# Performance work log

Measured on AMD Instinct MI355X. Metric: run time of the kernel, lower is better.

Reference implementation:

```python
import jax, jax.numpy as jnp
import numpy as np

B, T, D_IN, H, K, C = 8, 2048, 512, 384, 8192, 8
N_BLOCKS = 6
EPS = 1e-5


def conv1d(x, w, b, pad, groups=1):
    # x: [B, Cin, T], w: [Cout, Cin//groups, k]
    y = jax.lax.conv_general_dilated(
        x, w, window_strides=(1,), padding=[(pad, pad)],
        dimension_numbers=("NCH", "OIH", "NCH"), feature_group_count=groups)
    return y + b[None, :, None]


def layernorm(x, g, b):
    # normalize over last axis
    m = jnp.mean(x, axis=-1, keepdims=True)
    v = jnp.mean(jnp.square(x - m), axis=-1, keepdims=True)
    return (x - m) * jax.lax.rsqrt(v + EPS) * g + b


def setup_inputs() -> dict:
    key = jax.random.key(0)
    ks = iter(jax.random.split(key, 32))
    s = 0.02
    inp = {
        "x": jax.random.normal(next(ks), (B, T, D_IN), dtype=jnp.float32),
        "enc_w": jax.random.normal(next(ks), (H, D_IN, 7)) * s,
        "enc_b": jnp.zeros((H,)),
        "enc_ln_g": jnp.ones((H,)),
        "enc_ln_b": jnp.zeros((H,)),
        "blk_dw_w": jax.random.normal(next(ks), (N_BLOCKS, H, 1, 7)) * s,
        "blk_dw_b": jnp.zeros((N_BLOCKS, H)),
        "blk_ln_g": jnp.ones((N_BLOCKS, H)),
        "blk_ln_b": jnp.zeros((N_BLOCKS, H)),
        "blk_w1": jax.random.normal(next(ks), (N_BLOCKS, 4 * H, H)) * s,
        "blk_b1": jnp.zeros((N_BLOCKS, 4 * H)),
        "blk_w2": jax.random.normal(next(ks), (N_BLOCKS, H, 4 * H)) * s,
        "blk_b2": jnp.zeros((N_BLOCKS, H)),
        "out_w": jax.random.normal(next(ks), (C, H, 1)) * s,
        "out_b": jnp.zeros((C,)),
        "embeddings": jax.random.normal(next(ks), (K, C)),
    }
    return inp


def encode(x, enc_w, enc_b, enc_ln_g, enc_ln_b, blk_dw_w, blk_dw_b,
           blk_ln_g, blk_ln_b, blk_w1, blk_b1, blk_w2, blk_b2, out_w, out_b):
    h = x.transpose(0, 2, 1)                       # [B, D_IN, T]
    h = conv1d(h, enc_w, enc_b, pad=3)             # [B, H, T]
    h = layernorm(h.transpose(0, 2, 1), enc_ln_g, enc_ln_b).transpose(0, 2, 1)
    for i in range(N_BLOCKS):
        res = h
        h = conv1d(h, blk_dw_w[i], blk_dw_b[i], pad=3, groups=H)  # depthwise
        ht = h.transpose(0, 2, 1)                  # [B, T, H]
        ht = layernorm(ht, blk_ln_g[i], blk_ln_b[i])
        ht = jnp.einsum("bth,fh->btf", ht, blk_w1[i]) + blk_b1[i]
        ht = jax.nn.gelu(ht, approximate=False)    # torch GELU is exact erf
        ht = jnp.einsum("btf,hf->bth", ht, blk_w2[i]) + blk_b2[i]
        h = ht.transpose(0, 2, 1) + res
    z = conv1d(h, out_w, out_b, pad=0)             # [B, C, T]
    return z.transpose(0, 2, 1)                    # [B, T, C]


def reference(x, enc_w, enc_b, enc_ln_g, enc_ln_b, blk_dw_w, blk_dw_b,
              blk_ln_g, blk_ln_b, blk_w1, blk_b1, blk_w2, blk_b2,
              out_w, out_b, embeddings):
    z = encode(x, enc_w, enc_b, enc_ln_g, enc_ln_b, blk_dw_w, blk_dw_b,
               blk_ln_g, blk_ln_b, blk_w1, blk_b1, blk_w2, blk_b2, out_w, out_b)
    flat = z.reshape(-1, C)                        # [B*T, C]
    # squared euclidean distances: same argmin as torch.cdist
    d2 = (jnp.sum(flat * flat, axis=1, keepdims=True)
          - 2.0 * flat @ embeddings.T
          + jnp.sum(embeddings * embeddings, axis=1))  # [B*T, K]
    indices = jnp.argmin(d2, axis=1)               # [B*T], int
    return indices
```

## Files before the change

kernel.cpp:

```cpp
#include <hip/hip_runtime.h>
#include <math.h>

#define T_   2048
#define DIN  512
#define H_   384
#define H4_  1536
#define BT_  16384

typedef _Float16 half_t;
typedef _Float16 f16x8 __attribute__((ext_vector_type(8)));
typedef _Float16 f16x4 __attribute__((ext_vector_type(4)));
typedef float f32x4 __attribute__((ext_vector_type(4)));

#define LO_SCALE 2048.0f
#define LO_INV   4.8828125e-4f

__device__ __forceinline__ void gload_lds(const half_t* g, half_t* l) {
    __builtin_amdgcn_global_load_lds(
        (const __attribute__((address_space(1))) unsigned int*)(const void*)g,
        (__attribute__((address_space(3))) unsigned int*)(void*)l, 16, 0, 0);
}

__device__ __forceinline__ void split2(float v, half_t* hi, half_t* lo) {
    half_t h = (half_t)v;
    *hi = h;
    *lo = (half_t)((v - (float)h) * LO_SCALE);
}

__global__ void k_split4(const float* __restrict__ in, half_t* __restrict__ hi,
                         half_t* __restrict__ lo, long n4) {
    long i = (long)blockIdx.x * 256 + threadIdx.x;
    if (i >= n4) return;
    float4 v = ((const float4*)in)[i];
    f16x4 vh, vl;
    float a[4] = {v.x, v.y, v.z, v.w};
#pragma unroll
    for (int j = 0; j < 4; ++j) {
        half_t h = (half_t)a[j];
        vh[j] = h;
        vl[j] = (half_t)((a[j] - (float)h) * LO_SCALE);
    }
    ((f16x4*)hi)[i] = vh;
    ((f16x4*)lo)[i] = vl;
}

__global__ void k_split_pad(const float* __restrict__ in, half_t* __restrict__ hi,
                            half_t* __restrict__ lo) {
    long i = (long)blockIdx.x * 256 + threadIdx.x;
    if (i >= 2103296L) return;
    int ii4 = (int)(i & 127);
    long rest = i >> 7;
    int u = (int)(rest % 2054);
    int b = (int)(rest / 2054);
    f16x4 vh = (f16x4)(half_t)0.f, vl = (f16x4)(half_t)0.f;
    if (u >= 3 && u < 2051) {
        float4 v = ((const float4*)in)[((long)b * 2048 + (u - 3)) * 128 + ii4];
        float a[4] = {v.x, v.y, v.z, v.w};
#pragma unroll
        for (int j = 0; j < 4; ++j) {
            half_t h = (half_t)a[j];
            vh[j] = h;
            vl[j] = (half_t)((a[j] - (float)h) * LO_SCALE);
        }
    }
    ((f16x4*)hi)[i] = vh;
    ((f16x4*)lo)[i] = vl;
}

__global__ void k_split_encw(const float* __restrict__ in, half_t* __restrict__ hi,
                             half_t* __restrict__ lo) {
    int idx = blockIdx.x * 256 + threadIdx.x;
    if (idx >= H_ * 3584) return;
    int n = idx / 3584;
    int r = idx % 3584;
    int tap = r >> 9, i = r & 511;
    split2(in[n * 3584 + i * 7 + tap], hi + idx, lo + idx);
}

__global__ void k_ln(const float* __restrict__ in, float* __restrict__ out,
                     const float* __restrict__ g, const float* __restrict__ b) {
    int row = blockIdx.x;
    int lane = threadIdx.x;
    const float* ir = in + (long)row * H_;
    float v[6];
    float s = 0.f;
#pragma unroll
    for (int j = 0; j < 6; ++j) { v[j] = ir[lane + (j << 6)]; s += v[j]; }
#pragma unroll
    for (int o = 32; o > 0; o >>= 1) s += __shfl_down(s, o, 64);
    s = __shfl(s, 0, 64);
    float mean = s * (1.f / 384.f);
    float q = 0.f;
#pragma unroll
    for (int j = 0; j < 6; ++j) { float d = v[j] - mean; q += d * d; }
#pragma unroll
    for (int o = 32; o > 0; o >>= 1) q += __shfl_down(q, o, 64);
    q = __shfl(q, 0, 64);
    float rstd = rsqrtf(q * (1.f / 384.f) + 1e-5f);
    float* orow = out + (long)row * H_;
#pragma unroll
    for (int j = 0; j < 6; ++j) {
        int c = lane + (j << 6);
        orow[c] = (v[j] - mean) * rstd * g[c] + b[c];
    }
}

__global__ __launch_bounds__(256) void k_dwconv_ln(
    const float* __restrict__ h, half_t* __restrict__ oh,
    half_t* __restrict__ ol,
    const float* __restrict__ w, const float* __restrict__ wb,
    const float* __restrict__ g, const float* __restrict__ gb) {
    int row = (blockIdx.x << 2) + (threadIdx.x >> 6);
    int b = row >> 11;
    int t = row & 2047;
    int lane = threadIdx.x & 63;
    const float* hb = h + ((long)b * T_) * H_;
    float vx[3], vy[3];
    float s = 0.f;
#pragma unroll
    for (int j = 0; j < 3; ++j) {
        int c = (lane << 1) + (j << 7);
        float ax = wb[c], ay = wb[c + 1];
        const float* wcx = w + c * 7;
        const float* wcy = wcx + 7;
#pragma unroll
        for (int k = 0; k < 7; ++k) {
            int tt = t + k - 3;
            if ((unsigned)tt < (unsigned)T_) {
                float2 hv = *(const float2*)&hb[(long)tt * H_ + c];
                ax = fmaf(hv.x, wcx[k], ax);
                ay = fmaf(hv.y, wcy[k], ay);
            }
        }
        vx[j] = ax; vy[j] = ay;
        s += ax + ay;
    }
#pragma unroll
    for (int o = 32; o > 0; o >>= 1) s += __shfl_down(s, o, 64);
    s = __shfl(s, 0, 64);
    float mean = s * (1.f / 384.f);
    float q = 0.f;
#pragma unroll
    for (int j = 0; j < 3; ++j) {
        float dx = vx[j] - mean, dy = vy[j] - mean;
        q += dx * dx + dy * dy;
    }
#pragma unroll
    for (int o = 32; o > 0; o >>= 1) q += __shfl_down(q, o, 64);
    q = __shfl(q, 0, 64);
    float rstd = rsqrtf(q * (1.f / 384.f) + 1e-5f);
    long ro = (long)row * H_;
#pragma unroll
    for (int j = 0; j < 3; ++j) {
        int c = (lane << 1) + (j << 7);
        float valx = (vx[j] - mean) * rstd * g[c] + gb[c];
        float valy = (vy[j] - mean) * rstd * g[c + 1] + gb[c + 1];
        split2(valx, oh + ro + c, ol + ro + c);
        split2(valy, oh + ro + c + 1, ol + ro + c + 1);
    }
}

template <int MODE, int NT>
__global__ __launch_bounds__(512, 2) void k_g192p(
    const half_t* __restrict__ Ah, const half_t* __restrict__ Al,
    const half_t* __restrict__ Bh, const half_t* __restrict__ Bl,
    const float* __restrict__ bias, const float* __restrict__ res,
    float* __restrict__ Cf, half_t* __restrict__ Ch, half_t* __restrict__ Cl,
    int N, int K) {
    __shared__ __align__(16) half_t smem[61440];
    const int tid = threadIdx.x;
    const int lane = tid & 63, wid = tid >> 6;
    const int wm = (wid & 1) << 6;
    const int wn = ((wid >> 1) & 3) * 48;
    const int quad = lane >> 4, l16 = lane & 15;

    constexpr int NWG = 128 * NT;
    constexpr int CHUNK = NWG / 8;
    const int lin = blockIdx.x;
    const int tile = (lin & 7) * CHUNK + (lin >> 3);
    const int m0 = (tile / NT) << 7;
    const int n0 = (tile % NT) * 192;

    long abase;
    int astr;
    if (MODE == 0) {
        abase = (long)(m0 >> 11) * 2054 + (m0 & 2047);
        astr = 512;
    } else {
        abase = m0;
        astr = K;
    }

    const int lr = lane >> 2;
    const int lg = (lane & 3) ^ ((lane >> 3) & 3);
    const half_t* gsrc[5];
    int ldo[5];
#pragma unroll
    for (int j = 0; j < 5; ++j) {
        int q = wid * 5 + j;
        if (q < 8) {
            gsrc[j] = Ah + (abase + q * 16 + lr) * (long)astr + lg * 8;
            ldo[j] = q * 512;
        } else if (q < 16) {
            gsrc[j] = Al + (abase + (q - 8) * 16 + lr) * (long)astr + lg * 8;
            ldo[j] = 4096 + (q - 8) * 512;
        } else if (q < 28) {
            gsrc[j] = Bh + ((long)(n0 + (q - 16) * 16 + lr)) * K + lg * 8;
            ldo[j] = 8192 + (q - 16) * 512;
        } else {
            gsrc[j] = Bl + ((long)(n0 + (q - 28) * 16 + lr)) * K + lg * 8;
            ldo[j] = 14336 + (q - 28) * 512;
        }
    }

#define STAGE3(bufb, k0_) do {                                              \
    int k0v = (k0_);                                                        \
    _Pragma("unroll")                                                       \
    for (int j = 0; j < 5; ++j)                                             \
        gload_lds(gsrc[j] + k0v, &smem[(bufb) + ldo[j]]);                   \
} while (0)

    f32x4 acc1[4][3] = {};
    f32x4 acc2[4][3] = {};
    const int sw = ((quad ^ (l16 >> 1)) & 3) << 3;

    const int nIter = K >> 5;
    STAGE3(0, 0);
    STAGE3(20480, 32);
    int b0 = 0, b1 = 20480, b2 = 40960;
    for (int it = 0; it < nIter; ++it) {
        if (it + 1 < nIter)
            asm volatile("s_waitcnt vmcnt(5)" ::: "memory");
        else
            asm volatile("s_waitcnt vmcnt(0)" ::: "memory");
        __builtin_amdgcn_s_barrier();
        __builtin_amdgcn_sched_barrier(0);

        const int ab = b0 + (wm + l16) * 32 + sw;
        const int bb = b0 + 8192 + (wn + l16) * 32 + sw;
        const int k2 = (it + 2) << 5;
        const bool st = (it + 2 < nIter);
        f16x8 fah[4], fal[4], fgh[3], fgl[3];

#pragma unroll
        for (int f = 0; f < 4; ++f)
            fah[f] = *(const f16x8*)&smem[ab + f * 512];
#pragma unroll
        for (int g = 0; g < 3; ++g)
            fgl[g] = *(const f16x8*)&smem[bb + 6144 + g * 512];
        if (st) {
            gload_lds(gsrc[0] + k2, &smem[b2 + ldo[0]]);
            gload_lds(gsrc[1] + k2, &smem[b2 + ldo[1]]);
        }
        __builtin_amdgcn_s_setprio(1);
#pragma unroll
        for (int f = 0; f < 4; ++f)
#pragma unroll
            for (int g = 0; g < 3; ++g)
                acc2[f][g] = __builtin_amdgcn_mfma_f32_16x16x32_f16(fah[f], fgl[g], acc2[f][g], 0, 0, 0);
        __builtin_amdgcn_s_setprio(0);

#pragma unroll
        for (int f = 0; f < 4; ++f)
            fal[f] = *(const f16x8*)&smem[ab + 4096 + f * 512];
#pragma unroll
        for (int g = 0; g < 3; ++g)
            fgh[g] = *(const f16x8*)&smem[bb + g * 512];
        if (st) {
            gload_lds(gsrc[2] + k2, &smem[b2 + ldo[2]]);
            gload_lds(gsrc[3] + k2, &smem[b2 + ldo[3]]);
            gload_lds(gsrc[4] + k2, &smem[b2 + ldo[4]]);
        }
        __builtin_amdgcn_s_setprio(1);
#pragma unroll
        for (int f = 0; f < 4; ++f)
#pragma unroll
            for (int g = 0; g < 3; ++g)
                acc2[f][g] = __builtin_amdgcn_mfma_f32_16x16x32_f16(fal[f], fgh[g], acc2[f][g], 0, 0, 0);
        __builtin_amdgcn_s_setprio(0);

        __builtin_amdgcn_s_setprio(1);
#pragma unroll
        for (int f = 0; f < 4; ++f)
#pragma unroll
            for (int g = 0; g < 3; ++g)
                acc1[f][g] = __builtin_amdgcn_mfma_f32_16x16x32_f16(fah[f], fgh[g], acc1[f][g], 0, 0, 0);
        __builtin_amdgcn_s_setprio(0);

        int t_ = b0; b0 = b1; b1 = b2; b2 = t_;
    }
#undef STAGE3

    float bv[3];
#pragma unroll
    for (int g = 0; g < 3; ++g) bv[g] = bias[n0 + wn + g * 16 + l16];

    if (MODE == 1) {
        __syncthreads();
#pragma unroll
        for (int f = 0; f < 4; ++f)
#pragma unroll
            for (int g = 0; g < 3; ++g)
#pragma unroll
                for (int r = 0; r < 4; ++r) {
                    int rm = wm + f * 16 + quad * 4 + r;
                    int cn = wn + g * 16 + l16;
                    float v = acc1[f][g][r] + acc2[f][g][r] * LO_INV + bv[g];
                    v = 0.5f * v * (1.0f + erff(v * 0.70710678118654752f));
                    half_t hh = (half_t)v;
                    smem[rm * 200 + cn] = hh;
                    smem[25600 + rm * 200 + cn] = (half_t)((v - (float)hh) * LO_SCALE);
                }
        __syncthreads();
        int row = tid >> 2, c0 = (tid & 3) * 48;
        long go = (long)(m0 + row) * N + n0 + c0;
        int so = row * 200 + c0;
#pragma unroll
        for (int u = 0; u < 6; ++u) {
            *(float4*)(Ch + go + u * 8) = *(const float4*)&smem[so + u * 8];
            *(float4*)(Cl + go + u * 8) = *(const float4*)&smem[25600 + so + u * 8];
        }
    } else {
#pragma unroll
        for (int f = 0; f < 4; ++f)
#pragma unroll
            for (int g = 0; g < 3; ++g)
#pragma unroll
                for (int r = 0; r < 4; ++r) {
                    long row = m0 + wm + f * 16 + quad * 4 + r;
                    int col = n0 + wn + g * 16 + l16;
                    float v = acc1[f][g][r] + acc2[f][g][r] * LO_INV + bv[g];
                    long o = row * N + col;
                    if (MODE == 2) v += res[o];
                    Cf[o] = v;
                }
    }
}

__global__ __launch_bounds__(256) void k_outconv_argmin(
    const float* __restrict__ h, const float* __restrict__ ow,
    const float* __restrict__ ob, const float* __restrict__ emb,
    int* __restrict__ outIdx) {
    __shared__ float hs[16][H_ + 1];
    __shared__ float zs[16][8];
    __shared__ float es[16 * 516];
    __shared__ float rb[16][16];
    __shared__ int ri[16][16];
    const int tid = threadIdx.x;
    const int row0 = blockIdx.x << 4;

    for (int i = tid; i < 16 * (H_ / 4); i += 256) {
        int r = i / 96;
        int c4 = (i % 96) << 2;
        float4 v = *(const float4*)&h[((long)(row0 + r)) * H_ + c4];
        hs[r][c4] = v.x; hs[r][c4 + 1] = v.y; hs[r][c4 + 2] = v.z; hs[r][c4 + 3] = v.w;
    }
    __syncthreads();

    if (tid < 128) {
        int r = tid & 15, c = tid >> 4;
        float acc = ob[c];
        const float* wc = ow + c * H_;
        for (int j = 0; j < H_; ++j) acc = fmaf(hs[r][j], wc[j], acc);
        zs[r][c] = acc;
    }
    __syncthreads();

    const int r = tid & 15;
    const int sl = tid >> 4;
    float z0 = zs[r][0], z1 = zs[r][1], z2 = zs[r][2], z3 = zs[r][3];
    float z4 = zs[r][4], z5 = zs[r][5], z6 = zs[r][6], z7 = zs[r][7];
    float best = 3.4e38f;
    int bi = 0;

    for (int ch = 0; ch < 8; ++ch) {
        __syncthreads();
        for (int i = tid; i < 2048; i += 256) {
            int e = i >> 1;
            int half = (i & 1) << 2;
            float4 src = *(const float4*)&emb[(((long)(ch << 10)) + e) * 8 + half];
            *(float4*)&es[(e >> 6) * 516 + ((e & 63) << 3) + half] = src;
        }
        __syncthreads();
        const float* ep = es + sl * 516;
        int gbase = (ch << 10) + (sl << 6);
#pragma unroll 4
        for (int j = 0; j < 64; ++j) {
            float4 e0 = *(const float4*)(ep + (j << 3));
            float4 e1 = *(const float4*)(ep + (j << 3) + 4);
            float t, d;
            t = e0.x - z0; d = t * t;
            t = e0.y - z1; d = fmaf(t, t, d);
            t = e0.z - z2; d = fmaf(t, t, d);
            t = e0.w - z3; d = fmaf(t, t, d);
            t = e1.x - z4; d = fmaf(t, t, d);
            t = e1.y - z5; d = fmaf(t, t, d);
            t = e1.z - z6; d = fmaf(t, t, d);
            t = e1.w - z7; d = fmaf(t, t, d);
            if (d < best) { best = d; bi = gbase + j; }
        }
    }
    rb[r][sl] = best;
    ri[r][sl] = bi;
    __syncthreads();
    if (sl == 0) {
        float bb = rb[r][0];
        int bbi = ri[r][0];
#pragma unroll
        for (int s2 = 1; s2 < 16; ++s2) {
            float v = rb[r][s2];
            int i2 = ri[r][s2];
            if (v < bb || (v == bb && i2 < bbi)) { bb = v; bbi = i2; }
        }
        outIdx[row0 + r] = bbi;
    }
}

extern "C" void kernel_launch(void* const* d_in, const int* in_sizes, int n_in,
                              void* d_out, int out_size, void* d_ws, size_t ws_size,
                              hipStream_t stream) {
    const float* x        = (const float*)d_in[0];
    const float* enc_w    = (const float*)d_in[1];
    const float* enc_b    = (const float*)d_in[2];
    const float* enc_ln_g = (const float*)d_in[3];
    const float* enc_ln_b = (const float*)d_in[4];
    const float* blk_dw_w = (const float*)d_in[5];
    const float* blk_dw_b = (const float*)d_in[6];
    const float* blk_ln_g = (const float*)d_in[7];
    const float* blk_ln_b = (const float*)d_in[8];
    const float* blk_w1   = (const float*)d_in[9];
    const float* blk_b1   = (const float*)d_in[10];
    const float* blk_w2   = (const float*)d_in[11];
    const float* blk_b2   = (const float*)d_in[12];
    const float* out_w    = (const float*)d_in[13];
    const float* out_b    = (const float*)d_in[14];
    const float* emb      = (const float*)d_in[15];
    int* out = (int*)d_out;

    char* base = (char*)d_ws;
    float*  h    = (float*)base;
    half_t* tmph = (half_t*)(base + 25165824);
    half_t* tmpl = (half_t*)(base + 37748736);
    half_t* ht4h = (half_t*)(base + 50331648);
    half_t* ht4l = (half_t*)(base + 100663296);
    half_t* ench = (half_t*)(base + 150994944);
    half_t* encl = (half_t*)(base + 153747456);
    half_t* w1h  = (half_t*)(base + 156499968);
    half_t* w1l  = (half_t*)(base + 163577856);
    half_t* w2h  = (half_t*)(base + 170655744);
    half_t* w2l  = (half_t*)(base + 177733632);
    half_t* xph = (half_t*)(base + 50331648);
    half_t* xpl = (half_t*)(base + 50331648 + 16826368);

    k_split_pad<<<8216, 256, 0, stream>>>(x, xph, xpl);
    k_split4<<<3456, 256, 0, stream>>>(blk_w1, w1h, w1l, 884736L);
    k_split4<<<3456, 256, 0, stream>>>(blk_w2, w2h, w2l, 884736L);
    k_split_encw<<<(H_ * 3584 + 255) / 256, 256, 0, stream>>>(enc_w, ench, encl);

    k_g192p<0, 2><<<256, 512, 0, stream>>>(xph, xpl, ench, encl, enc_b,
                                           nullptr, h, nullptr, nullptr,
                                           H_, 3584);
    k_ln<<<BT_, 64, 0, stream>>>(h, h, enc_ln_g, enc_ln_b);

    for (int i = 0; i < 6; ++i) {
        k_dwconv_ln<<<BT_ / 4, 256, 0, stream>>>(h, tmph, tmpl, blk_dw_w + i * H_ * 7,
                                                 blk_dw_b + i * H_, blk_ln_g + i * H_,
                                                 blk_ln_b + i * H_);
        k_g192p<1, 8><<<1024, 512, 0, stream>>>(
            tmph, tmpl, w1h + (long)i * 589824, w1l + (long)i * 589824,
            blk_b1 + i * H4_, nullptr, nullptr, ht4h, ht4l, H4_, H_);
        k_g192p<2, 2><<<256, 512, 0, stream>>>(
            ht4h, ht4l, w2h + (long)i * 589824, w2l + (long)i * 589824,
            blk_b2 + i * H_, h, h, nullptr, nullptr, H_, H4_);
    }

    k_outconv_argmin<<<BT_ / 16, 256, 0, stream>>>(h, out_w, out_b, emb, out);
}
```

Before: 1.647 ms.

## Stage GEMM epilogue through LDS, stagger wave LDS reads, batch LN rows

The fp32 GEMM epilogue (modes 0 and 2) now writes accumulators to padded LDS, then each thread stores 48 contiguous floats with float4 writes and float4 residual reads, replacing scattered per-element global accesses. The second group of waves reverses the order of its hi/lo fragment loads inside the main loop, which is meant to spread LDS bank and port pressure across waves. The standalone layernorm kernel now handles four rows per 256-thread block instead of one row per 64-thread block. The epilogue adds two barriers and reuses LDS that the pipeline also uses.

```diff
diff --git a/kernel.cpp b/kernel.cpp
--- a/kernel.cpp
+++ b/kernel.cpp
@@ -77,10 +77,11 @@
     split2(in[n * 3584 + i * 7 + tap], hi + idx, lo + idx);
 }
 
-__global__ void k_ln(const float* __restrict__ in, float* __restrict__ out,
-                     const float* __restrict__ g, const float* __restrict__ b) {
-    int row = blockIdx.x;
-    int lane = threadIdx.x;
+__global__ __launch_bounds__(256) void k_ln(
+    const float* __restrict__ in, float* __restrict__ out,
+    const float* __restrict__ g, const float* __restrict__ b) {
+    int row = (blockIdx.x << 2) + (threadIdx.x >> 6);
+    int lane = threadIdx.x & 63;
     const float* ir = in + (long)row * H_;
     float v[6];
     float s = 0.f;
@@ -159,6 +160,57 @@
         split2(valy, oh + ro + c + 1, ol + ro + c + 1);
     }
 }
+
+#define KHALF1(AOFF, BOFF, F1A, F1B)                                        \
+    _Pragma("unroll")                                                       \
+    for (int f = 0; f < 4; ++f)                                             \
+        F1A[f] = *(const f16x8*)&smem[ab + (AOFF) + f * 512];               \
+    _Pragma("unroll")                                                       \
+    for (int g = 0; g < 3; ++g)                                             \
+        F1B[g] = *(const f16x8*)&smem[bb + (BOFF) + g * 512];               \
+    if (st) {                                                               \
+        gload_lds(gsrc[0] + k2, &smem[b2 + ldo[0]]);                        \
+        gload_lds(gsrc[1] + k2, &smem[b2 + ldo[1]]);                        \
+    }                                                                       \
+    __builtin_amdgcn_s_setprio(1);                                          \
+    _Pragma("unroll")                                                       \
+    for (int f = 0; f < 4; ++f)                                             \
+        _Pragma("unroll")                                                   \
+        for (int g = 0; g < 3; ++g)                                         \
+            acc2[f][g] = __builtin_amdgcn_mfma_f32_16x16x32_f16(            \
+                F1A[f], F1B[g], acc2[f][g], 0, 0, 0);                       \
+    __builtin_amdgcn_s_setprio(0);
+
+#define KHALF2(AOFF, BOFF, F2A, F2B)                                        \
+    _Pragma("unroll")                                                       \
+    for (int f = 0; f < 4; ++f)                                             \
+        F2A[f] = *(const f16x8*)&smem[ab + (AOFF) + f * 512];               \
+    _Pragma("unroll")                                                       \
+    for (int g = 0; g < 3; ++g)                                             \
+        F2B[g] = *(const f16x8*)&smem[bb + (BOFF) + g * 512];               \
+    if (st) {                                                               \
+        gload_lds(gsrc[2] + k2, &smem[b2 + ldo[2]]);                        \
+        gload_lds(gsrc[3] + k2, &smem[b2 + ldo[3]]);                        \
+        gload_lds(gsrc[4] + k2, &smem[b2 + ldo[4]]);                        \
+    }                                                                       \
+    __builtin_amdgcn_s_setprio(1);                                          \
+    _Pragma("unroll")                                                       \
+    for (int f = 0; f < 4; ++f)                                             \
+        _Pragma("unroll")                                                   \
+        for (int g = 0; g < 3; ++g)                                         \
+            acc2[f][g] = __builtin_amdgcn_mfma_f32_16x16x32_f16(            \
+                F2A[f], F2B[g], acc2[f][g], 0, 0, 0);                       \
+    __builtin_amdgcn_s_setprio(0);
+
+#define KHI(FAH, FGH)                                                       \
+    __builtin_amdgcn_s_setprio(1);                                          \
+    _Pragma("unroll")                                                       \
+    for (int f = 0; f < 4; ++f)                                             \
+        _Pragma("unroll")                                                   \
+        for (int g = 0; g < 3; ++g)                                         \
+            acc1[f][g] = __builtin_amdgcn_mfma_f32_16x16x32_f16(            \
+                FAH[f], FGH[g], acc1[f][g], 0, 0, 0);                       \
+    __builtin_amdgcn_s_setprio(0);
 
 template <int MODE, int NT>
 __global__ __launch_bounds__(512, 2) void k_g192p(
@@ -173,6 +225,7 @@
     const int wm = (wid & 1) << 6;
     const int wn = ((wid >> 1) & 3) * 48;
     const int quad = lane >> 4, l16 = lane & 15;
+    const bool flip = (wid >> 2) & 1;
 
     constexpr int NWG = 128 * NT;
     constexpr int CHUNK = NWG / 8;
@@ -240,52 +293,18 @@
         const int bb = b0 + 8192 + (wn + l16) * 32 + sw;
         const int k2 = (it + 2) << 5;
         const bool st = (it + 2 < nIter);
-        f16x8 fah[4], fal[4], fgh[3], fgl[3];
-
-#pragma unroll
-        for (int f = 0; f < 4; ++f)
-            fah[f] = *(const f16x8*)&smem[ab + f * 512];
-#pragma unroll
-        for (int g = 0; g < 3; ++g)
-            fgl[g] = *(const f16x8*)&smem[bb + 6144 + g * 512];
-        if (st) {
-            gload_lds(gsrc[0] + k2, &smem[b2 + ldo[0]]);
-            gload_lds(gsrc[1] + k2, &smem[b2 + ldo[1]]);
-        }
-        __builtin_amdgcn_s_setprio(1);
-#pragma unroll
-        for (int f = 0; f < 4; ++f)
-#pragma unroll
-            for (int g = 0; g < 3; ++g)
-                acc2[f][g] = __builtin_amdgcn_mfma_f32_16x16x32_f16(fah[f], fgl[g], acc2[f][g], 0, 0, 0);
-        __builtin_amdgcn_s_setprio(0);
-
-#pragma unroll
-        for (int f = 0; f < 4; ++f)
-            fal[f] = *(const f16x8*)&smem[ab + 4096 + f * 512];
-#pragma unroll
-        for (int g = 0; g < 3; ++g)
-            fgh[g] = *(const f16x8*)&smem[bb + g * 512];
-        if (st) {
-            gload_lds(gsrc[2] + k2, &smem[b2 + ldo[2]]);
-            gload_lds(gsrc[3] + k2, &smem[b2 + ldo[3]]);
-            gload_lds(gsrc[4] + k2, &smem[b2 + ldo[4]]);
-        }
-        __builtin_amdgcn_s_setprio(1);
-#pragma unroll
-        for (int f = 0; f < 4; ++f)
-#pragma unroll
-            for (int g = 0; g < 3; ++g)
-                acc2[f][g] = __builtin_amdgcn_mfma_f32_16x16x32_f16(fal[f], fgh[g], acc2[f][g], 0, 0, 0);
-        __builtin_amdgcn_s_setprio(0);
-
-        __builtin_amdgcn_s_setprio(1);
-#pragma unroll
-        for (int f = 0; f < 4; ++f)
-#pragma unroll
-            for (int g = 0; g < 3; ++g)
-                acc1[f][g] = __builtin_amdgcn_mfma_f32_16x16x32_f16(fah[f], fgh[g], acc1[f][g], 0, 0, 0);
-        __builtin_amdgcn_s_setprio(0);
+
+        if (!flip) {
+            f16x8 f1a[4], f1b[3], f2a[4], f2b[3];
+            KHALF1(0, 6144, f1a, f1b)
+            KHALF2(4096, 0, f2a, f2b)
+            KHI(f1a, f2b)
+        } else {
+            f16x8 f1a[4], f1b[3], f2a[4], f2b[3];
+            KHALF1(4096, 0, f1a, f1b)
+            KHALF2(0, 6144, f2a, f2b)
+            KHI(f2a, f1b)
+        }
 
         int t_ = b0; b0 = b1; b1 = b2; b2 = t_;
     }
@@ -321,19 +340,32 @@
             *(float4*)(Cl + go + u * 8) = *(const float4*)&smem[25600 + so + u * 8];
         }
     } else {
+        __syncthreads();
+        float* smemf = (float*)smem;
 #pragma unroll
         for (int f = 0; f < 4; ++f)
 #pragma unroll
             for (int g = 0; g < 3; ++g)
 #pragma unroll
                 for (int r = 0; r < 4; ++r) {
-                    long row = m0 + wm + f * 16 + quad * 4 + r;
-                    int col = n0 + wn + g * 16 + l16;
-                    float v = acc1[f][g][r] + acc2[f][g][r] * LO_INV + bv[g];
-                    long o = row * N + col;
-                    if (MODE == 2) v += res[o];
-                    Cf[o] = v;
+                    int rm = wm + f * 16 + quad * 4 + r;
+                    int cn = wn + g * 16 + l16;
+                    smemf[rm * 196 + cn] =
+                        acc1[f][g][r] + acc2[f][g][r] * LO_INV + bv[g];
                 }
+        __syncthreads();
+        int row = tid >> 2, c0 = (tid & 3) * 48;
+        long go = (long)(m0 + row) * N + n0 + c0;
+        int so = row * 196 + c0;
+#pragma unroll
+        for (int u = 0; u < 12; ++u) {
+            float4 v = *(const float4*)&smemf[so + u * 4];
+            if (MODE == 2) {
+                float4 rr = *(const float4*)(res + go + u * 4);
+                v.x += rr.x; v.y += rr.y; v.z += rr.z; v.w += rr.w;
+            }
+            *(float4*)(Cf + go + u * 4) = v;
+        }
     }
 }
 
@@ -460,7 +492,7 @@
     k_g192p<0, 2><<<256, 512, 0, stream>>>(xph, xpl, ench, encl, enc_b,
                                            nullptr, h, nullptr, nullptr,
                                            H_, 3584);
-    k_ln<<<BT_, 64, 0, stream>>>(h, h, enc_ln_g, enc_ln_b);
+    k_ln<<<BT_ / 4, 256, 0, stream>>>(h, h, enc_ln_g, enc_ln_b);
 
     for (int i = 0; i < 6; ++i) {
         k_dwconv_ln<<<BT_ / 4, 256, 0, stream>>>(h, tmph, tmpl, blk_dw_w + i * H_ * 7,
```

New measurement: 1.639 ms. About the same (-0.5%).
